# Performance work log

Hardware: AMD Instinct MI355X
Metric: run time of the kernel (lower is better)

The kernel has to match this reference:

```python
import jax, jax.numpy as jnp
import numpy as np


def setup_inputs() -> dict:
    key = jax.random.key(0)
    k1, k2, k3, k4 = jax.random.split(key, 4)
    B, S, E, H = 8, 2048, 1024, 64
    x = jax.random.normal(k1, (B, S, E), dtype=jnp.float32)
    scale = 1.0 / np.sqrt(E)
    Wq = jax.random.normal(k2, (E, H), dtype=jnp.float32) * scale
    Wk = jax.random.normal(k3, (E, H), dtype=jnp.float32) * scale
    Wv = jax.random.normal(k4, (E, H), dtype=jnp.float32) * scale
    return {"x": x, "Wq": Wq, "Wk": Wk, "Wv": Wv}


def reference(x, Wq, Wk, Wv):
    # x: [B, S, E]; Wq/Wk/Wv: [E, H]
    B, S, E = x.shape
    H = Wq.shape[1]
    q = x @ Wq  # [B, S, H]
    k = x @ Wk
    v = x @ Wv
    inv_sqrt_h = 1.0 / jnp.sqrt(jnp.asarray(H, dtype=x.dtype))
    att = jnp.einsum("bqh,bkh->bqk", q, k) * inv_sqrt_h  # [B, S, S]
    causal = jnp.tril(jnp.ones((S, S), dtype=bool))
    att = jnp.where(causal, att, jnp.asarray(-jnp.inf, dtype=att.dtype))
    att = jax.nn.softmax(att, axis=-1)
    # dropout p=0.0 (eval) -> identity
    return jnp.einsum("bqk,bkh->bqh", att, v)  # [B, S, H]
```

## Files before the change

kernel.cpp:

```cpp
#include <hip/hip_runtime.h>
#include <math.h>

typedef __attribute__((ext_vector_type(8))) short bf16x8;
typedef __attribute__((ext_vector_type(16))) float fx16;

#define SEQ 2048
#define HD 64

__device__ __forceinline__ unsigned f2bf_bits(float f){
  unsigned u = __float_as_uint(f);
  return (u + 0x7fffu + ((u >> 16) & 1u)) >> 16;
}
__device__ __forceinline__ unsigned cvt_pk_bf16(float a, float b){
  unsigned r;
  asm("v_cvt_pk_bf16_f32 %0, %1, %2" : "=v"(r) : "v"(a), "v"(b));
  return r;
}
union U8 { bf16x8 v; short s[8]; unsigned u[4]; };

__device__ __forceinline__ fx16 mfma_bf16(bf16x8 a, bf16x8 b, fx16 c){
  return __builtin_amdgcn_mfma_f32_32x32x16_bf16(a, b, c, 0, 0, 0);
}
__device__ __forceinline__ fx16 fzero(){
  fx16 z;
#pragma unroll
  for (int i = 0; i < 16; ++i) z[i] = 0.f;
  return z;
}

__global__ __launch_bounds__(256) void wconv_kernel(
    const float* __restrict__ Wq, const float* __restrict__ Wk, const float* __restrict__ Wv,
    short* __restrict__ wsB)
{
  int gid = blockIdx.x * 4 + (threadIdx.x >> 6);
  int lane = threadIdx.x & 63;
  int l31 = lane & 31, h = lane >> 5;
  int half = gid & 1;
  int rem = gid >> 1;
  int t = rem % 6;
  int stage = rem / 6;
  int n = t * 32 + l31;
  int mat = n >> 6, col = n & 63;
  const float* W = (mat == 0) ? Wq : (mat == 1) ? Wk : Wv;
  int kbase = stage * 16 + h * 8;
  U8 o;
#pragma unroll
  for (int i = 0; i < 8; ++i) {
    float f = W[(size_t)(kbase + i) * 64 + col];
    unsigned hb = f2bf_bits(f);
    if (half == 0) o.s[i] = (short)hb;
    else {
      float hf = __uint_as_float(hb << 16);
      o.s[i] = (short)f2bf_bits(f - hf);
    }
  }
  *(bf16x8*)(wsB + (size_t)gid * 512 + lane * 8) = o.v;
}

__global__ __launch_bounds__(256, 2) void proj_kernel(
    const float* __restrict__ x, const short* __restrict__ wsB,
    short* __restrict__ qh, short* __restrict__ ql,
    short* __restrict__ kh, short* __restrict__ kl,
    short* __restrict__ vth, short* __restrict__ vtl)
{
  __shared__ float Vb[64 * 68];

  const int tid = threadIdx.x;
  const int lane = tid & 63, w = tid >> 6;
  const int l31 = lane & 31, h = lane >> 5;
  const int m = w & 1;
  const int nset = (w >> 1) * 3;
  const int row0 = blockIdx.x * 64;
  const size_t xrow = (size_t)(row0 + m * 32 + l31) * 1024;

  fx16 accP[3], accQ[3];
#pragma unroll
  for (int t = 0; t < 3; ++t) { accP[t] = fzero(); accQ[t] = fzero(); }

  float4 A0[4][2], A1[4][2];
  bf16x8 B0[6], B1[6];

#define LOADA(AB, C1)                                                   \
  {                                                                     \
    _Pragma("unroll")                                                   \
    for (int ks = 0; ks < 4; ++ks) {                                    \
      int k = (C1) * 64 + ks * 16 + h * 8;                              \
      AB[ks][0] = *(const float4*)(x + xrow + k);                       \
      AB[ks][1] = *(const float4*)(x + xrow + k + 4);                   \
    }                                                                   \
  }

#define LOADB(BB, SR)                                                   \
  {                                                                     \
    _Pragma("unroll")                                                   \
    for (int tt = 0; tt < 3; ++tt) {                                    \
      size_t g2 = ((size_t)(SR) * 6 + nset + tt) * 2;                   \
      BB[tt * 2 + 0] = *(const bf16x8*)(wsB + g2 * 512 + lane * 8);     \
      BB[tt * 2 + 1] = *(const bf16x8*)(wsB + (g2 + 1) * 512 + lane * 8);\
    }                                                                   \
  }

#define STEP(AF, BB)                                                    \
  {                                                                     \
    U8 ah, al;                                                          \
    float xf[8];                                                        \
    xf[0] = AF[0].x; xf[1] = AF[0].y; xf[2] = AF[0].z; xf[3] = AF[0].w; \
    xf[4] = AF[1].x; xf[5] = AF[1].y; xf[6] = AF[1].z; xf[7] = AF[1].w; \
    _Pragma("unroll")                                                   \
    for (int i = 0; i < 8; ++i) {                                       \
      unsigned hb = f2bf_bits(xf[i]);                                   \
      ah.s[i] = (short)hb;                                              \
      float hf = __uint_as_float(hb << 16);                             \
      al.s[i] = (short)f2bf_bits(xf[i] - hf);                           \
    }                                                                   \
    _Pragma("unroll")                                                   \
    for (int tt = 0; tt < 3; ++tt) {                                    \
      accP[tt] = mfma_bf16(ah.v, BB[tt * 2 + 0], accP[tt]);             \
      accQ[tt] = mfma_bf16(ah.v, BB[tt * 2 + 1], accQ[tt]);             \
      accQ[tt] = mfma_bf16(al.v, BB[tt * 2 + 0], accQ[tt]);             \
    }                                                                   \
  }

#define CHUNK(C, ACUR, ANEXT)                                           \
  {                                                                     \
    if ((C) < 15) LOADA(ANEXT, (C) + 1);                                \
    STEP(ACUR[0], B0); if ((C) * 4 + 2 < 64) LOADB(B0, (C) * 4 + 2);    \
    STEP(ACUR[1], B1); if ((C) * 4 + 3 < 64) LOADB(B1, (C) * 4 + 3);    \
    STEP(ACUR[2], B0); if ((C) * 4 + 4 < 64) LOADB(B0, (C) * 4 + 4);    \
    STEP(ACUR[3], B1); if ((C) * 4 + 5 < 64) LOADB(B1, (C) * 4 + 5);    \
  }

  LOADA(A0, 0);
  LOADB(B0, 0);
  LOADB(B1, 1);
  for (int c2 = 0; c2 < 8; ++c2) {
    CHUNK(2 * c2 + 0, A0, A1);
    CHUNK(2 * c2 + 1, A1, A0);
  }
#undef CHUNK
#undef STEP
#undef LOADB
#undef LOADA

#pragma unroll
  for (int t = 0; t < 3; ++t) {
    int nt = nset + t;
    int mat = nt >> 1;
    int colb = (nt & 1) * 32 + l31;
    if (mat < 2) {
      short* dh = (mat == 0) ? qh : kh;
      short* dl = (mat == 0) ? ql : kl;
#pragma unroll
      for (int r = 0; r < 16; ++r) {
        float f = accP[t][r] + accQ[t][r];
        int rowg = row0 + m * 32 + (r & 3) + 8 * (r >> 2) + 4 * h;
        unsigned hb = f2bf_bits(f);
        float hf = __uint_as_float(hb << 16);
        unsigned lb = f2bf_bits(f - hf);
        dh[(size_t)rowg * 64 + colb] = (short)hb;
        dl[(size_t)rowg * 64 + colb] = (short)lb;
      }
    } else {
#pragma unroll
      for (int r = 0; r < 16; ++r) {
        float f = accP[t][r] + accQ[t][r];
        int srel = m * 32 + (r & 3) + 8 * (r >> 2) + 4 * h;
        Vb[srel * 68 + (nt - 4) * 32 + l31] = f;
      }
    }
  }
  __syncthreads();
  {
    int d = tid >> 2, sc = (tid & 3) * 16;
    int bb = row0 >> 11, s0 = row0 & 2047;
    U8 hv0, hv1, lv0, lv1;
#pragma unroll
    for (int ss = 0; ss < 16; ++ss) {
      float f = Vb[(sc + ss) * 68 + d];
      unsigned hb = f2bf_bits(f);
      float hf = __uint_as_float(hb << 16);
      unsigned lb = f2bf_bits(f - hf);
      if (ss < 8) { hv0.s[ss] = (short)hb; lv0.s[ss] = (short)lb; }
      else        { hv1.s[ss - 8] = (short)hb; lv1.s[ss - 8] = (short)lb; }
    }
    size_t o = (size_t)(bb * 64 + d) * 2048 + s0 + sc;
    *(bf16x8*)(vth + o) = hv0.v;  *(bf16x8*)(vth + o + 8) = hv1.v;
    *(bf16x8*)(vtl + o) = lv0.v;  *(bf16x8*)(vtl + o + 8) = lv1.v;
  }
}

__global__ __launch_bounds__(256, 2) void attn_kernel(
    const short* __restrict__ qh, const short* __restrict__ ql,
    const short* __restrict__ kh, const short* __restrict__ kl,
    const short* __restrict__ vth, const short* __restrict__ vtl,
    float* __restrict__ segO, float* __restrict__ segL, float* __restrict__ segM)
{
  __shared__ short Kbuf[2][64 * 128];
  __shared__ short Vbuf[2][64 * 128];

  const int bid = blockIdx.x;
  const int b = bid / 40;
  const int j = bid % 40;
  int qt, ch, nch;
  if (j < 4)       { nch = 1; qt = j;               ch = 0; }
  else if (j < 12) { nch = 2; qt = 4 + (j - 4) / 2; ch = (j - 4) % 2; }
  else if (j < 24) { nch = 3; qt = 8 + (j - 12) / 3; ch = (j - 12) % 3; }
  else             { nch = 4; qt = 12 + (j - 24) / 4; ch = (j - 24) % 4; }
  const int S = 2 * qt + 2;
  const int bs = S / nch, rem = S % nch;
  const int nsteps = bs + (ch < rem ? 1 : 0);
  const int kt0 = ch * bs + (ch < rem ? ch : rem);

  const int tid = threadIdx.x;
  const int lane = tid & 63, w = tid >> 6;
  const int l31 = lane & 31, h = lane >> 5;
  const int qabs = qt * 128 + w * 32 + l31;

  bf16x8 qf0[4], qf1[4];
  {
    size_t qrow = ((size_t)b * 2048 + qabs) * 64;
#pragma unroll
    for (int ds = 0; ds < 4; ++ds) {
      qf0[ds] = *(const bf16x8*)(qh + qrow + ds * 16 + 8 * h);
      qf1[ds] = *(const bf16x8*)(ql + qrow + ds * 16 + 8 * h);
    }
  }

  const int slot = tid & 15;
  const int half = slot >> 3;
  const int sb = (slot & 7) << 4;
  const int rbase = tid >> 4;
  const int d0 = (sb ^ ((rbase & 7) << 4)) >> 1;
  const short* ksrc = half ? kl : kh;
  const short* vsrc = half ? vtl : vth;
  const int woff = rbase * 256 + half * 128 + sb;

  fx16 accA0 = fzero(), accA1 = fzero(), accB0 = fzero(), accB1 = fzero();
  float Mrun = -3e38f, lrun = 0.f;
  const int sw = (l31 & 7) << 4;

  bf16x8 kreg[4], vreg[4];
#pragma unroll
  for (int jj = 0; jj < 4; ++jj) {
    kreg[jj] = *(const bf16x8*)(ksrc + ((size_t)b * 2048 + (size_t)kt0 * 64 + rbase + 16 * jj) * 64 + d0);
    vreg[jj] = *(const bf16x8*)(vsrc + ((size_t)(b * 64 + rbase + 16 * jj)) * 2048 + kt0 * 64 + d0);
  }
#pragma unroll
  for (int jj = 0; jj < 4; ++jj) {
    *(bf16x8*)((char*)Kbuf[0] + woff + jj * 4096) = kreg[jj];
    *(bf16x8*)((char*)Vbuf[0] + woff + jj * 4096) = vreg[jj];
  }
  __syncthreads();

  for (int it = 0; it < nsteps; ++it) {
    const int kt = kt0 + it;
    const int p = it & 1;
    const bool hasnext = (it + 1 < nsteps);
    if (hasnext) {
      int kn = kt + 1;
#pragma unroll
      for (int jj = 0; jj < 4; ++jj) {
        kreg[jj] = *(const bf16x8*)(ksrc + ((size_t)b * 2048 + (size_t)kn * 64 + rbase + 16 * jj) * 64 + d0);
        vreg[jj] = *(const bf16x8*)(vsrc + ((size_t)(b * 64 + rbase + 16 * jj)) * 2048 + kn * 64 + d0);
      }
    }

#pragma unroll
    for (int ms = 0; ms < 2; ++ms) {
      fx16 stA = fzero(), stB = fzero(), stC = fzero();
      {
        const char* arow = (const char*)Kbuf[p] + (ms * 32 + l31) * 256;
#pragma unroll
        for (int ds = 0; ds < 4; ++ds) {
          const int kb = ds * 32 + 16 * h;
          bf16x8 ah = *(const bf16x8*)(arow + (kb ^ sw));
          bf16x8 al = *(const bf16x8*)(arow + 128 + (kb ^ sw));
          stA = mfma_bf16(ah, qf0[ds], stA);
          stB = mfma_bf16(ah, qf1[ds], stB);
          stC = mfma_bf16(al, qf0[ds], stC);
        }
      }
      float sv[16];
      const int kbase = kt * 64 + ms * 32;
      const bool diag = (kbase + 31 > qt * 128 + w * 32);
#pragma unroll
      for (int r = 0; r < 16; ++r) {
        float s = (stA[r] + stB[r] + stC[r]) * 0.125f;
        if (diag) {
          int ka = kbase + (r & 3) + 8 * (r >> 2) + 4 * h;
          if (ka > qabs) s = -3e38f;
        }
        sv[r] = s;
      }
      float tm = sv[0];
#pragma unroll
      for (int r = 1; r < 16; ++r) tm = fmaxf(tm, sv[r]);
      tm = fmaxf(tm, __shfl_xor(tm, 32, 64));
      float Mnew = fmaxf(Mrun, tm);
      float alpha = __expf(Mrun - Mnew);
      Mrun = Mnew;
      float pvv[16]; float psum = 0.f;
#pragma unroll
      for (int r = 0; r < 16; ++r) { pvv[r] = __expf(sv[r] - Mnew); psum += pvv[r]; }
      psum += __shfl_xor(psum, 32, 64);
      lrun = lrun * alpha + psum;
#pragma unroll
      for (int r = 0; r < 16; ++r) {
        accA0[r] *= alpha; accA1[r] *= alpha; accB0[r] *= alpha; accB1[r] *= alpha;
      }
      unsigned chv[8], clv[8];
#pragma unroll
      for (int q2 = 0; q2 < 8; ++q2) {
        unsigned c = cvt_pk_bf16(pvv[2 * q2], pvv[2 * q2 + 1]);
        chv[q2] = c;
        float f0 = __uint_as_float(c << 16);
        float f1 = __uint_as_float(c & 0xffff0000u);
        clv[q2] = cvt_pk_bf16(pvv[2 * q2] - f0, pvv[2 * q2 + 1] - f1);
      }
#pragma unroll
      for (int kp = 0; kp < 2; ++kp) {
        U8 ph, pl;
        {
          unsigned c0 = chv[4 * kp], c1 = chv[4 * kp + 1], c2 = chv[4 * kp + 2], c3 = chv[4 * kp + 3];
          unsigned x0 = (unsigned)__shfl_xor((int)c0, 32, 64);
          unsigned x1 = (unsigned)__shfl_xor((int)c1, 32, 64);
          unsigned x2 = (unsigned)__shfl_xor((int)c2, 32, 64);
          unsigned x3 = (unsigned)__shfl_xor((int)c3, 32, 64);
          ph.u[0] = h ? x2 : c0;  ph.u[1] = h ? x3 : c1;
          ph.u[2] = h ? c2 : x0;  ph.u[3] = h ? c3 : x1;
          c0 = clv[4 * kp]; c1 = clv[4 * kp + 1]; c2 = clv[4 * kp + 2]; c3 = clv[4 * kp + 3];
          x0 = (unsigned)__shfl_xor((int)c0, 32, 64);
          x1 = (unsigned)__shfl_xor((int)c1, 32, 64);
          x2 = (unsigned)__shfl_xor((int)c2, 32, 64);
          x3 = (unsigned)__shfl_xor((int)c3, 32, 64);
          pl.u[0] = h ? x2 : c0;  pl.u[1] = h ? x3 : c1;
          pl.u[2] = h ? c2 : x0;  pl.u[3] = h ? c3 : x1;
        }
        const int kbv = ms * 64 + kp * 32 + 16 * h;
#pragma unroll
        for (int md = 0; md < 2; ++md) {
          const char* vrow = (const char*)Vbuf[p] + (md * 32 + l31) * 256;
          bf16x8 vh = *(const bf16x8*)(vrow + (kbv ^ sw));
          bf16x8 vl = *(const bf16x8*)(vrow + 128 + (kbv ^ sw));
          if (md == 0) {
            accA0 = mfma_bf16(vh, ph.v, accA0);
            accB0 = mfma_bf16(vh, pl.v, accB0);
            accB0 = mfma_bf16(vl, ph.v, accB0);
          } else {
            accA1 = mfma_bf16(vh, ph.v, accA1);
            accB1 = mfma_bf16(vh, pl.v, accB1);
            accB1 = mfma_bf16(vl, ph.v, accB1);
          }
        }
      }
    }

    if (hasnext) {
#pragma unroll
      for (int jj = 0; jj < 4; ++jj) {
        *(bf16x8*)((char*)Kbuf[p ^ 1] + woff + jj * 4096) = kreg[jj];
        *(bf16x8*)((char*)Vbuf[p ^ 1] + woff + jj * 4096) = vreg[jj];
      }
    }
    __syncthreads();
  }

  float* o = segO + (size_t)bid * (64 * 128);
#pragma unroll
  for (int md = 0; md < 2; ++md) {
#pragma unroll
    for (int r = 0; r < 16; ++r) {
      int d = md * 32 + (r & 3) + 8 * (r >> 2) + 4 * h;
      float val = md ? (accA1[r] + accB1[r]) : (accA0[r] + accB0[r]);
      o[d * 128 + w * 32 + l31] = val;
    }
  }
  if (h == 0) {
    segL[(size_t)bid * 128 + w * 32 + l31] = lrun;
    segM[(size_t)bid * 128 + w * 32 + l31] = Mrun;
  }
}

__global__ __launch_bounds__(256) void combine_kernel(
    const float* __restrict__ segO, const float* __restrict__ segL,
    const float* __restrict__ segM, float* __restrict__ out)
{
  __shared__ float Sc[4][128];
  __shared__ float Linv[128];
  __shared__ float Ot[64 * 132];

  const int bq = blockIdx.x;
  const int b = bq >> 4, qt = bq & 15;
  const int g = qt >> 2, nch = g + 1;
  const int base = (g == 0) ? qt
                 : (g == 1) ? 4 + (qt - 4) * 2
                 : (g == 2) ? 12 + (qt - 8) * 3
                 : 24 + (qt - 12) * 4;
  const int slot0 = b * 40 + base;
  const int tid = threadIdx.x;

  if (tid < 128) {
    const int q = tid;
    float M = -3e38f;
    for (int c = 0; c < nch; ++c)
      M = fmaxf(M, segM[(size_t)(slot0 + c) * 128 + q]);
    float L = 0.f;
    for (int c = 0; c < nch; ++c) {
      float s = __expf(segM[(size_t)(slot0 + c) * 128 + q] - M);
      Sc[c][q] = s;
      L += s * segL[(size_t)(slot0 + c) * 128 + q];
    }
    Linv[q] = 1.f / L;
  }
  __syncthreads();
  {
    const int dr = tid >> 5;
    const int qc = (tid & 31) * 4;
    for (int dd = dr; dd < 64; dd += 8) {
      float4 acc = {0.f, 0.f, 0.f, 0.f};
      for (int c = 0; c < nch; ++c) {
        float4 v = *(const float4*)(segO + (size_t)(slot0 + c) * 8192 + dd * 128 + qc);
        acc.x += Sc[c][qc + 0] * v.x;
        acc.y += Sc[c][qc + 1] * v.y;
        acc.z += Sc[c][qc + 2] * v.z;
        acc.w += Sc[c][qc + 3] * v.w;
      }
      *(float4*)&Ot[dd * 132 + qc] = acc;
    }
  }
  __syncthreads();
  {
    const int q = tid >> 1, dh = (tid & 1) * 32;
    const float inv = Linv[q];
    float* dst = out + ((size_t)b * 2048 + qt * 128 + q) * 64 + dh;
#pragma unroll
    for (int i = 0; i < 8; ++i) {
      float4 o;
      o.x = Ot[(dh + 4 * i + 0) * 132 + q] * inv;
      o.y = Ot[(dh + 4 * i + 1) * 132 + q] * inv;
      o.z = Ot[(dh + 4 * i + 2) * 132 + q] * inv;
      o.w = Ot[(dh + 4 * i + 3) * 132 + q] * inv;
      *(float4*)(dst + 4 * i) = o;
    }
  }
}

extern "C" void kernel_launch(void* const* d_in, const int* in_sizes, int n_in,
                              void* d_out, int out_size, void* d_ws, size_t ws_size,
                              hipStream_t stream) {
  const float* x  = (const float*)d_in[0];
  const float* Wq = (const float*)d_in[1];
  const float* Wk = (const float*)d_in[2];
  const float* Wv = (const float*)d_in[3];

  char* wsb = (char*)d_ws;
  short* wsB = (short*)(wsb + 0);
  short* qh  = (short*)(wsb + 786432);
  short* ql  = (short*)(wsb + 2883584);
  short* kh  = (short*)(wsb + 4980736);
  short* kl  = (short*)(wsb + 7077888);
  short* vth = (short*)(wsb + 9175040);
  short* vtl = (short*)(wsb + 11272192);
  float* segO = (float*)(wsb + 13369344);
  float* segL = (float*)(wsb + 23855104);
  float* segM = (float*)(wsb + 24018944);

  wconv_kernel<<<192, 256, 0, stream>>>(Wq, Wk, Wv, wsB);
  proj_kernel<<<256, 256, 0, stream>>>(x, wsB, qh, ql, kh, kl, vth, vtl);
  attn_kernel<<<320, 256, 0, stream>>>(qh, ql, kh, kl, vth, vtl, segO, segL, segM);
  combine_kernel<<<128, 256, 0, stream>>>(segO, segL, segM, (float*)d_out);
}
```

Baseline: 99.05 us.

## Split projection over K halves and rebalance attention into fixed 4-tile chunks

```diff
diff --git a/kernel.cpp b/kernel.cpp
--- a/kernel.cpp
+++ b/kernel.cpp
@@ -57,34 +57,36 @@
   *(bf16x8*)(wsB + (size_t)gid * 512 + lane * 8) = o.v;
 }
 
-__global__ __launch_bounds__(256, 2) void proj_kernel(
+__global__ __launch_bounds__(384, 3) void proj_kernel(
     const float* __restrict__ x, const short* __restrict__ wsB,
     short* __restrict__ qh, short* __restrict__ ql,
     short* __restrict__ kh, short* __restrict__ kl,
     short* __restrict__ vth, short* __restrict__ vtl)
 {
-  __shared__ float Vb[64 * 68];
+  __shared__ float Rx[6 * 64 * 17];
+  __shared__ float Vb[32 * 68];
 
   const int tid = threadIdx.x;
   const int lane = tid & 63, w = tid >> 6;
   const int l31 = lane & 31, h = lane >> 5;
-  const int m = w & 1;
-  const int nset = (w >> 1) * 3;
-  const int row0 = blockIdx.x * 64;
-  const size_t xrow = (size_t)(row0 + m * 32 + l31) * 1024;
-
-  fx16 accP[3], accQ[3];
-#pragma unroll
-  for (int t = 0; t < 3; ++t) { accP[t] = fzero(); accQ[t] = fzero(); }
+  const int ksel = (w >= 3) ? 1 : 0;
+  const int tp = w - ksel * 3;
+  const int row0 = blockIdx.x * 32;
+  const size_t xrow = (size_t)(row0 + l31) * 1024;
+  const int sbase = ksel * 32;
+
+  fx16 accP[2], accQ[2];
+#pragma unroll
+  for (int t = 0; t < 2; ++t) { accP[t] = fzero(); accQ[t] = fzero(); }
 
   float4 A0[4][2], A1[4][2];
-  bf16x8 B0[6], B1[6];
+  bf16x8 B0[4], B1[4];
 
 #define LOADA(AB, C1)                                                   \
   {                                                                     \
     _Pragma("unroll")                                                   \
     for (int ks = 0; ks < 4; ++ks) {                                    \
-      int k = (C1) * 64 + ks * 16 + h * 8;                              \
+      int k = ksel * 512 + (C1) * 64 + ks * 16 + h * 8;                 \
       AB[ks][0] = *(const float4*)(x + xrow + k);                       \
       AB[ks][1] = *(const float4*)(x + xrow + k + 4);                   \
     }                                                                   \
@@ -93,8 +95,8 @@
 #define LOADB(BB, SR)                                                   \
   {                                                                     \
     _Pragma("unroll")                                                   \
-    for (int tt = 0; tt < 3; ++tt) {                                    \
-      size_t g2 = ((size_t)(SR) * 6 + nset + tt) * 2;                   \
+    for (int tt = 0; tt < 2; ++tt) {                                    \
+      size_t g2 = ((size_t)(SR) * 6 + tp * 2 + tt) * 2;                 \
       BB[tt * 2 + 0] = *(const bf16x8*)(wsB + g2 * 512 + lane * 8);     \
       BB[tt * 2 + 1] = *(const bf16x8*)(wsB + (g2 + 1) * 512 + lane * 8);\
     }                                                                   \
@@ -114,7 +116,7 @@
       al.s[i] = (short)f2bf_bits(xf[i] - hf);                           \
     }                                                                   \
     _Pragma("unroll")                                                   \
-    for (int tt = 0; tt < 3; ++tt) {                                    \
+    for (int tt = 0; tt < 2; ++tt) {                                    \
       accP[tt] = mfma_bf16(ah.v, BB[tt * 2 + 0], accP[tt]);             \
       accQ[tt] = mfma_bf16(ah.v, BB[tt * 2 + 1], accQ[tt]);             \
       accQ[tt] = mfma_bf16(al.v, BB[tt * 2 + 0], accQ[tt]);             \
@@ -123,17 +125,17 @@
 
 #define CHUNK(C, ACUR, ANEXT)                                           \
   {                                                                     \
-    if ((C) < 15) LOADA(ANEXT, (C) + 1);                                \
-    STEP(ACUR[0], B0); if ((C) * 4 + 2 < 64) LOADB(B0, (C) * 4 + 2);    \
-    STEP(ACUR[1], B1); if ((C) * 4 + 3 < 64) LOADB(B1, (C) * 4 + 3);    \
-    STEP(ACUR[2], B0); if ((C) * 4 + 4 < 64) LOADB(B0, (C) * 4 + 4);    \
-    STEP(ACUR[3], B1); if ((C) * 4 + 5 < 64) LOADB(B1, (C) * 4 + 5);    \
+    if ((C) < 7) LOADA(ANEXT, (C) + 1);                                 \
+    STEP(ACUR[0], B0); if ((C) * 4 + 2 < 32) LOADB(B0, sbase + (C) * 4 + 2); \
+    STEP(ACUR[1], B1); if ((C) * 4 + 3 < 32) LOADB(B1, sbase + (C) * 4 + 3); \
+    STEP(ACUR[2], B0); if ((C) * 4 + 4 < 32) LOADB(B0, sbase + (C) * 4 + 4); \
+    STEP(ACUR[3], B1); if ((C) * 4 + 5 < 32) LOADB(B1, sbase + (C) * 4 + 5); \
   }
 
   LOADA(A0, 0);
-  LOADB(B0, 0);
-  LOADB(B1, 1);
-  for (int c2 = 0; c2 < 8; ++c2) {
+  LOADB(B0, sbase + 0);
+  LOADB(B1, sbase + 1);
+  for (int c2 = 0; c2 < 4; ++c2) {
     CHUNK(2 * c2 + 0, A0, A1);
     CHUNK(2 * c2 + 1, A1, A0);
   }
@@ -142,50 +144,59 @@
 #undef LOADB
 #undef LOADA
 
-#pragma unroll
-  for (int t = 0; t < 3; ++t) {
-    int nt = nset + t;
-    int mat = nt >> 1;
-    int colb = (nt & 1) * 32 + l31;
-    if (mat < 2) {
-      short* dh = (mat == 0) ? qh : kh;
-      short* dl = (mat == 0) ? ql : kl;
-#pragma unroll
-      for (int r = 0; r < 16; ++r) {
-        float f = accP[t][r] + accQ[t][r];
-        int rowg = row0 + m * 32 + (r & 3) + 8 * (r >> 2) + 4 * h;
-        unsigned hb = f2bf_bits(f);
-        float hf = __uint_as_float(hb << 16);
-        unsigned lb = f2bf_bits(f - hf);
-        dh[(size_t)rowg * 64 + colb] = (short)hb;
-        dl[(size_t)rowg * 64 + colb] = (short)lb;
-      }
-    } else {
-#pragma unroll
-      for (int r = 0; r < 16; ++r) {
-        float f = accP[t][r] + accQ[t][r];
-        int srel = m * 32 + (r & 3) + 8 * (r >> 2) + 4 * h;
-        Vb[srel * 68 + (nt - 4) * 32 + l31] = f;
-      }
-    }
+  if (ksel == 1) {
+#pragma unroll
+    for (int t = 0; t < 2; ++t)
+#pragma unroll
+      for (int r = 0; r < 16; ++r)
+        Rx[((tp * 2 + t) * 64 + lane) * 17 + r] = accP[t][r] + accQ[t][r];
   }
   __syncthreads();
-  {
-    int d = tid >> 2, sc = (tid & 3) * 16;
+  if (ksel == 0) {
+#pragma unroll
+    for (int t = 0; t < 2; ++t) {
+      const int tg = tp * 2 + t;
+      const int mat = tg >> 1;
+      const int colb = (tg & 1) * 32 + l31;
+      if (mat < 2) {
+        short* dh = (mat == 0) ? qh : kh;
+        short* dl = (mat == 0) ? ql : kl;
+#pragma unroll
+        for (int r = 0; r < 16; ++r) {
+          float f = accP[t][r] + accQ[t][r] + Rx[(tg * 64 + lane) * 17 + r];
+          int rowg = row0 + (r & 3) + 8 * (r >> 2) + 4 * h;
+          unsigned hb = f2bf_bits(f);
+          float hf = __uint_as_float(hb << 16);
+          unsigned lb = f2bf_bits(f - hf);
+          dh[(size_t)rowg * 64 + colb] = (short)hb;
+          dl[(size_t)rowg * 64 + colb] = (short)lb;
+        }
+      } else {
+#pragma unroll
+        for (int r = 0; r < 16; ++r) {
+          float f = accP[t][r] + accQ[t][r] + Rx[(tg * 64 + lane) * 17 + r];
+          int srel = (r & 3) + 8 * (r >> 2) + 4 * h;
+          Vb[srel * 68 + (tg - 4) * 32 + l31] = f;
+        }
+      }
+    }
+  }
+  __syncthreads();
+  if (tid < 256) {
+    int d = tid >> 2, s8 = (tid & 3) * 8;
     int bb = row0 >> 11, s0 = row0 & 2047;
-    U8 hv0, hv1, lv0, lv1;
-#pragma unroll
-    for (int ss = 0; ss < 16; ++ss) {
-      float f = Vb[(sc + ss) * 68 + d];
+    U8 hv, lv;
+#pragma unroll
+    for (int ss = 0; ss < 8; ++ss) {
+      float f = Vb[(s8 + ss) * 68 + d];
       unsigned hb = f2bf_bits(f);
       float hf = __uint_as_float(hb << 16);
-      unsigned lb = f2bf_bits(f - hf);
-      if (ss < 8) { hv0.s[ss] = (short)hb; lv0.s[ss] = (short)lb; }
-      else        { hv1.s[ss - 8] = (short)hb; lv1.s[ss - 8] = (short)lb; }
-    }
-    size_t o = (size_t)(bb * 64 + d) * 2048 + s0 + sc;
-    *(bf16x8*)(vth + o) = hv0.v;  *(bf16x8*)(vth + o + 8) = hv1.v;
-    *(bf16x8*)(vtl + o) = lv0.v;  *(bf16x8*)(vtl + o + 8) = lv1.v;
+      hv.s[ss] = (short)hb;
+      lv.s[ss] = (short)f2bf_bits(f - hf);
+    }
+    size_t o = (size_t)(bb * 64 + d) * 2048 + s0 + s8;
+    *(bf16x8*)(vth + o) = hv.v;
+    *(bf16x8*)(vtl + o) = lv.v;
   }
 }
 
@@ -199,17 +210,18 @@
   __shared__ short Vbuf[2][64 * 128];
 
   const int bid = blockIdx.x;
-  const int b = bid / 40;
-  const int j = bid % 40;
-  int qt, ch, nch;
-  if (j < 4)       { nch = 1; qt = j;               ch = 0; }
-  else if (j < 12) { nch = 2; qt = 4 + (j - 4) / 2; ch = (j - 4) % 2; }
-  else if (j < 24) { nch = 3; qt = 8 + (j - 12) / 3; ch = (j - 12) % 3; }
-  else             { nch = 4; qt = 12 + (j - 24) / 4; ch = (j - 24) % 4; }
-  const int S = 2 * qt + 2;
-  const int bs = S / nch, rem = S % nch;
-  const int nsteps = bs + (ch < rem ? 1 : 0);
-  const int kt0 = ch * bs + (ch < rem ? ch : rem);
+  const int b = bid & 7;
+  int r = bid >> 3;
+  int qt = 0;
+  {
+    int acc = 0;
+    while (r >= acc + ((qt + 2) >> 1)) { acc += (qt + 2) >> 1; ++qt; }
+    r -= acc;
+  }
+  const int ch = r;
+  const int St = 2 * (qt + 1);
+  const int kt0 = 4 * ch;
+  int nsteps = St - kt0; if (nsteps > 4) nsteps = 4;
 
   const int tid = threadIdx.x;
   const int lane = tid & 63, w = tid >> 6;
@@ -270,6 +282,7 @@
       fx16 stA = fzero(), stB = fzero(), stC = fzero();
       {
         const char* arow = (const char*)Kbuf[p] + (ms * 32 + l31) * 256;
+        __builtin_amdgcn_s_setprio(1);
 #pragma unroll
         for (int ds = 0; ds < 4; ++ds) {
           const int kb = ds * 32 + 16 * h;
@@ -279,34 +292,35 @@
           stB = mfma_bf16(ah, qf1[ds], stB);
           stC = mfma_bf16(al, qf0[ds], stC);
         }
+        __builtin_amdgcn_s_setprio(0);
       }
       float sv[16];
       const int kbase = kt * 64 + ms * 32;
       const bool diag = (kbase + 31 > qt * 128 + w * 32);
 #pragma unroll
-      for (int r = 0; r < 16; ++r) {
-        float s = (stA[r] + stB[r] + stC[r]) * 0.125f;
+      for (int rr = 0; rr < 16; ++rr) {
+        float s = (stA[rr] + stB[rr] + stC[rr]) * 0.125f;
         if (diag) {
-          int ka = kbase + (r & 3) + 8 * (r >> 2) + 4 * h;
+          int ka = kbase + (rr & 3) + 8 * (rr >> 2) + 4 * h;
           if (ka > qabs) s = -3e38f;
         }
-        sv[r] = s;
+        sv[rr] = s;
       }
       float tm = sv[0];
 #pragma unroll
-      for (int r = 1; r < 16; ++r) tm = fmaxf(tm, sv[r]);
+      for (int rr = 1; rr < 16; ++rr) tm = fmaxf(tm, sv[rr]);
       tm = fmaxf(tm, __shfl_xor(tm, 32, 64));
       float Mnew = fmaxf(Mrun, tm);
       float alpha = __expf(Mrun - Mnew);
       Mrun = Mnew;
       float pvv[16]; float psum = 0.f;
 #pragma unroll
-      for (int r = 0; r < 16; ++r) { pvv[r] = __expf(sv[r] - Mnew); psum += pvv[r]; }
+      for (int rr = 0; rr < 16; ++rr) { pvv[rr] = __expf(sv[rr] - Mnew); psum += pvv[rr]; }
       psum += __shfl_xor(psum, 32, 64);
       lrun = lrun * alpha + psum;
 #pragma unroll
-      for (int r = 0; r < 16; ++r) {
-        accA0[r] *= alpha; accA1[r] *= alpha; accB0[r] *= alpha; accB1[r] *= alpha;
+      for (int rr = 0; rr < 16; ++rr) {
+        accA0[rr] *= alpha; accA1[rr] *= alpha; accB0[rr] *= alpha; accB1[rr] *= alpha;
       }
       unsigned chv[8], clv[8];
 #pragma unroll
@@ -337,6 +351,7 @@
           pl.u[2] = h ? c2 : x0;  pl.u[3] = h ? c3 : x1;
         }
         const int kbv = ms * 64 + kp * 32 + 16 * h;
+        __builtin_amdgcn_s_setprio(1);
 #pragma unroll
         for (int md = 0; md < 2; ++md) {
           const char* vrow = (const char*)Vbuf[p] + (md * 32 + l31) * 256;
@@ -352,6 +367,7 @@
             accB1 = mfma_bf16(vl, ph.v, accB1);
           }
         }
+        __builtin_amdgcn_s_setprio(0);
       }
     }
 
@@ -369,9 +385,9 @@
 #pragma unroll
   for (int md = 0; md < 2; ++md) {
 #pragma unroll
-    for (int r = 0; r < 16; ++r) {
-      int d = md * 32 + (r & 3) + 8 * (r >> 2) + 4 * h;
-      float val = md ? (accA1[r] + accB1[r]) : (accA0[r] + accB0[r]);
+    for (int rr = 0; rr < 16; ++rr) {
+      int d = md * 32 + (rr & 3) + 8 * (rr >> 2) + 4 * h;
+      float val = md ? (accA1[rr] + accB1[rr]) : (accA0[rr] + accB0[rr]);
       o[d * 128 + w * 32 + l31] = val;
     }
   }
@@ -385,30 +401,27 @@
     const float* __restrict__ segO, const float* __restrict__ segL,
     const float* __restrict__ segM, float* __restrict__ out)
 {
-  __shared__ float Sc[4][128];
+  __shared__ float Sc[8][128];
   __shared__ float Linv[128];
   __shared__ float Ot[64 * 132];
 
   const int bq = blockIdx.x;
   const int b = bq >> 4, qt = bq & 15;
-  const int g = qt >> 2, nch = g + 1;
-  const int base = (g == 0) ? qt
-                 : (g == 1) ? 4 + (qt - 4) * 2
-                 : (g == 2) ? 12 + (qt - 8) * 3
-                 : 24 + (qt - 12) * 4;
-  const int slot0 = b * 40 + base;
+  const int nch = (qt + 2) >> 1;
+  int U = 0;
+  for (int i = 0; i < qt; ++i) U += (i + 2) >> 1;
   const int tid = threadIdx.x;
 
   if (tid < 128) {
     const int q = tid;
     float M = -3e38f;
     for (int c = 0; c < nch; ++c)
-      M = fmaxf(M, segM[(size_t)(slot0 + c) * 128 + q]);
+      M = fmaxf(M, segM[(size_t)(b + 8 * (U + c)) * 128 + q]);
     float L = 0.f;
     for (int c = 0; c < nch; ++c) {
-      float s = __expf(segM[(size_t)(slot0 + c) * 128 + q] - M);
+      float s = __expf(segM[(size_t)(b + 8 * (U + c)) * 128 + q] - M);
       Sc[c][q] = s;
-      L += s * segL[(size_t)(slot0 + c) * 128 + q];
+      L += s * segL[(size_t)(b + 8 * (U + c)) * 128 + q];
     }
     Linv[q] = 1.f / L;
   }
@@ -419,7 +432,7 @@
     for (int dd = dr; dd < 64; dd += 8) {
       float4 acc = {0.f, 0.f, 0.f, 0.f};
       for (int c = 0; c < nch; ++c) {
-        float4 v = *(const float4*)(segO + (size_t)(slot0 + c) * 8192 + dd * 128 + qc);
+        float4 v = *(const float4*)(segO + (size_t)(b + 8 * (U + c)) * 8192 + dd * 128 + qc);
         acc.x += Sc[c][qc + 0] * v.x;
         acc.y += Sc[c][qc + 1] * v.y;
         acc.z += Sc[c][qc + 2] * v.z;
@@ -462,11 +475,11 @@
   short* vth = (short*)(wsb + 9175040);
   short* vtl = (short*)(wsb + 11272192);
   float* segO = (float*)(wsb + 13369344);
-  float* segL = (float*)(wsb + 23855104);
-  float* segM = (float*)(wsb + 24018944);
+  float* segL = (float*)(wsb + 32243712);
+  float* segM = (float*)(wsb + 32538624);
 
   wconv_kernel<<<192, 256, 0, stream>>>(Wq, Wk, Wv, wsB);
-  proj_kernel<<<256, 256, 0, stream>>>(x, wsB, qh, ql, kh, kl, vth, vtl);
-  attn_kernel<<<320, 256, 0, stream>>>(qh, ql, kh, kl, vth, vtl, segO, segL, segM);
+  proj_kernel<<<512, 384, 0, stream>>>(x, wsB, qh, ql, kh, kl, vth, vtl);
+  attn_kernel<<<576, 256, 0, stream>>>(qh, ql, kh, kl, vth, vtl, segO, segL, segM);
   combine_kernel<<<128, 256, 0, stream>>>(segO, segL, segM, (float*)d_out);
 }
```

New measurement: 123.6 us. 24.8% more time.
